# Optimization experiments

Hardware: AMD Instinct MI355X
Metric: run time of the kernel (lower is better)

## Reference

```python
import jax, jax.numpy as jnp
import numpy as np

N_NODES = 50000
N_EDGES = 800000
IN_DIM = 256
OUT_DIM = 256


def setup_inputs() -> dict:
    key = jax.random.key(0)
    k1, k2, k3, k4 = jax.random.split(key, 4)
    feature = jax.random.normal(k1, (N_NODES, IN_DIM), dtype=jnp.float32)
    weight = jax.random.normal(k2, (IN_DIM, OUT_DIM), dtype=jnp.float32)
    src = jax.random.randint(k3, (N_EDGES,), 0, N_NODES, dtype=jnp.int32)
    dst = jax.random.randint(k4, (N_EDGES,), 0, N_NODES, dtype=jnp.int32)
    return {"feature": feature, "weight": weight, "src": src, "dst": dst}


def reference(feature, weight, src, dst):
    # Kernel math: for each edge (s -> d): out[d] += feature[s] @ W.
    # By linearity this equals segment_sum(feature[src] by dst) @ W,
    # which avoids materializing the [E, OUT_DIM] transformed edge features.
    agg = jax.ops.segment_sum(feature[src], dst, num_segments=N_NODES)  # [N, in_dim]
    out = agg @ weight  # [N, out_dim]
    return out
```

## Files before the change

kernel.cpp:

```cpp
#include <hip/hip_runtime.h>
#include <hip/hip_bf16.h>

#define IN_DIM 256
#define OUT_DIM 256
#define CAP 64

typedef __attribute__((ext_vector_type(8))) short bf16x8;
typedef __attribute__((ext_vector_type(4))) float f32x4;


__global__ void feat2bf16(const float* __restrict__ f, unsigned short* __restrict__ o, int n) {
    int i = (blockIdx.x * blockDim.x + threadIdx.x) * 4;
    if (i < n) {
        float4 v = *(const float4*)(f + i);
        __hip_bfloat16 a = __float2bfloat16(v.x), b = __float2bfloat16(v.y);
        __hip_bfloat16 c = __float2bfloat16(v.z), d = __float2bfloat16(v.w);
        ushort4 u;
        u.x = *(unsigned short*)&a; u.y = *(unsigned short*)&b;
        u.z = *(unsigned short*)&c; u.w = *(unsigned short*)&d;
        *(ushort4*)(o + i) = u;
    }
}


__global__ void bucket_kernel(const int* __restrict__ src, const int* __restrict__ dst,
                              int* __restrict__ cursor, int* __restrict__ bucket, int E) {
    int e = blockIdx.x * blockDim.x + threadIdx.x;
    if (e < E) {
        int d = dst[e];
        int pos = atomicAdd(&cursor[d], 1);
        if (pos < CAP) bucket[d * CAP + pos] = src[e];
    }
}


__device__ inline float4 bf4_to_f4(ushort4 u) {
    float4 r;
    r.x = __uint_as_float((unsigned)u.x << 16);
    r.y = __uint_as_float((unsigned)u.y << 16);
    r.z = __uint_as_float((unsigned)u.z << 16);
    r.w = __uint_as_float((unsigned)u.w << 16);
    return r;
}

__global__ void aggregate_bf16(const unsigned short* __restrict__ feat,
                               const int* __restrict__ bucket, const int* __restrict__ cursor,
                               unsigned short* __restrict__ agg, int N) {
    int node = blockIdx.x * 4 + (threadIdx.x >> 6);
    int lane = threadIdx.x & 63;
    if (node >= N) return;
    int cnt = min(cursor[node], CAP);
    const int* bp = bucket + node * CAP;
    float4 a0 = make_float4(0.f,0.f,0.f,0.f), a1 = a0, a2 = a0, a3 = a0;
    int e = 0;
    for (; e + 4 <= cnt; e += 4) {
        int s0 = bp[e], s1 = bp[e+1], s2 = bp[e+2], s3 = bp[e+3];
        ushort4 u0 = ((const ushort4*)(feat + (size_t)s0 * IN_DIM))[lane];
        ushort4 u1 = ((const ushort4*)(feat + (size_t)s1 * IN_DIM))[lane];
        ushort4 u2 = ((const ushort4*)(feat + (size_t)s2 * IN_DIM))[lane];
        ushort4 u3 = ((const ushort4*)(feat + (size_t)s3 * IN_DIM))[lane];
        float4 v0 = bf4_to_f4(u0), v1 = bf4_to_f4(u1), v2 = bf4_to_f4(u2), v3 = bf4_to_f4(u3);
        a0.x += v0.x; a0.y += v0.y; a0.z += v0.z; a0.w += v0.w;
        a1.x += v1.x; a1.y += v1.y; a1.z += v1.z; a1.w += v1.w;
        a2.x += v2.x; a2.y += v2.y; a2.z += v2.z; a2.w += v2.w;
        a3.x += v3.x; a3.y += v3.y; a3.z += v3.z; a3.w += v3.w;
    }
    for (; e < cnt; ++e) {
        int s = bp[e];
        float4 v = bf4_to_f4(((const ushort4*)(feat + (size_t)s * IN_DIM))[lane]);
        a0.x += v.x; a0.y += v.y; a0.z += v.z; a0.w += v.w;
    }
    a0.x += a1.x + a2.x + a3.x;
    a0.y += a1.y + a2.y + a3.y;
    a0.z += a1.z + a2.z + a3.z;
    a0.w += a1.w + a2.w + a3.w;
    __hip_bfloat16 hx = __float2bfloat16(a0.x), hy = __float2bfloat16(a0.y);
    __hip_bfloat16 hz = __float2bfloat16(a0.z), hw = __float2bfloat16(a0.w);
    ushort4 o;
    o.x = *(unsigned short*)&hx; o.y = *(unsigned short*)&hy;
    o.z = *(unsigned short*)&hz; o.w = *(unsigned short*)&hw;
    ((ushort4*)(agg + (size_t)node * IN_DIM))[lane] = o;
}


__global__ void prep_w(const float* __restrict__ W, unsigned short* __restrict__ Wt) {
    int n = blockIdx.x, k = threadIdx.x;
    __hip_bfloat16 h = __float2bfloat16(W[k * OUT_DIM + n]);
    Wt[n * IN_DIM + k] = *(unsigned short*)&h;
}


__global__ __launch_bounds__(256) void gemm_mfma(const unsigned short* __restrict__ A,
                                                 const unsigned short* __restrict__ Bt,
                                                 float* __restrict__ C, int M) {
    __shared__ unsigned short sA[64][40];
    __shared__ unsigned short sB[128][40];
    int tid = threadIdx.x;
    int wave = tid >> 6, lane = tid & 63;
    int m16 = lane & 15, quad = lane >> 4;
    int rb = blockIdx.y * 64, cb = blockIdx.x * 128;
    f32x4 acc[8] = {};

    for (int k0 = 0; k0 < IN_DIM; k0 += 32) {
        {
            int r = tid >> 2, g = tid & 3;
            int gr = rb + r;
            ulonglong2 v; v.x = 0; v.y = 0;
            if (gr < M) v = *(const ulonglong2*)(A + (size_t)gr * IN_DIM + k0 + g * 8);
            *(ulonglong2*)&sA[r][g * 8] = v;
        }
        #pragma unroll
        for (int t = 0; t < 2; ++t) {
            int f = tid + t * 256;
            int nrow = f >> 2, g = f & 3;
            *(ulonglong2*)&sB[nrow][g * 8] =
                *(const ulonglong2*)(Bt + (size_t)(cb + nrow) * IN_DIM + k0 + g * 8);
        }
        __syncthreads();
        bf16x8 afrag = *(const bf16x8*)&sA[wave * 16 + m16][quad * 8];
        #pragma unroll
        for (int nt = 0; nt < 8; ++nt) {
            bf16x8 bfrag = *(const bf16x8*)&sB[nt * 16 + m16][quad * 8];
            acc[nt] = __builtin_amdgcn_mfma_f32_16x16x32_bf16(afrag, bfrag, acc[nt], 0, 0, 0);
        }
        __syncthreads();
    }
    #pragma unroll
    for (int nt = 0; nt < 8; ++nt) {
        #pragma unroll
        for (int r = 0; r < 4; ++r) {
            int gr = rb + wave * 16 + quad * 4 + r;
            if (gr < M) C[(size_t)gr * OUT_DIM + cb + nt * 16 + m16] = acc[nt][r];
        }
    }
}


extern "C" void kernel_launch(void* const* d_in, const int* in_sizes, int n_in,
                              void* d_out, int out_size, void* d_ws, size_t ws_size,
                              hipStream_t stream) {
    const float* feature = (const float*)d_in[0];
    const float* weight  = (const float*)d_in[1];
    const int*   src     = (const int*)d_in[2];
    const int*   dst     = (const int*)d_in[3];
    float*       out     = (float*)d_out;

    int N = in_sizes[0] / IN_DIM;
    int E = in_sizes[2];
    int nfeat = N * IN_DIM;

    char* ws = (char*)d_ws;
    size_t halfTab = (size_t)N * IN_DIM * sizeof(unsigned short);
    unsigned short* agg   = (unsigned short*)ws;
    unsigned short* featb = (unsigned short*)(ws + halfTab);
    unsigned short* Wt    = (unsigned short*)(ws + 2 * halfTab);
    char* p = ws + 2 * halfTab + (size_t)IN_DIM * OUT_DIM * sizeof(unsigned short);
    int* cursor = (int*)p;
    int* bucket = cursor + N;

    hipMemsetAsync(cursor, 0, (size_t)N * sizeof(int), stream);

    feat2bf16<<<(nfeat / 4 + 255) / 256, 256, 0, stream>>>(feature, featb, nfeat);
    prep_w<<<OUT_DIM, IN_DIM, 0, stream>>>(weight, Wt);
    bucket_kernel<<<(E + 255) / 256, 256, 0, stream>>>(src, dst, cursor, bucket, E);
    aggregate_bf16<<<(N + 3) / 4, 256, 0, stream>>>(featb, bucket, cursor, agg, N);

    dim3 ggrid(OUT_DIM / 128, (N + 63) / 64);
    gemm_mfma<<<ggrid, 256, 0, stream>>>(agg, Wt, out, N);
}
```

Before: 224.5 us.

## Fuse prep kernels and column-slice aggregation with 16-bit bucket indices

Merges feature conversion, weight transpose and edge bucketing into one launch, pads per-node cursors to separate cache lines to reduce atomic contention, and stores source indices as 16-bit values. Aggregation now splits the 256 columns into 8 slices of 32, with lane groups striding over edges and a shuffle reduction, so that each slice's gather footprint can stay resident in cache. The 16-bit indices assume fewer than 65536 nodes, and the padded cursor array enlarges the memset.

```diff
diff --git a/kernel.cpp b/kernel.cpp
--- a/kernel.cpp
+++ b/kernel.cpp
@@ -4,89 +4,87 @@
 #define IN_DIM 256
 #define OUT_DIM 256
 #define CAP 64
+#define NS 8
+#define SW 32
 
 typedef __attribute__((ext_vector_type(8))) short bf16x8;
 typedef __attribute__((ext_vector_type(4))) float f32x4;
 
+__device__ inline unsigned short bfbits(float x) {
+    __hip_bfloat16 h = __float2bfloat16(x);
+    return *(unsigned short*)&h;
+}
 
-__global__ void feat2bf16(const float* __restrict__ f, unsigned short* __restrict__ o, int n) {
-    int i = (blockIdx.x * blockDim.x + threadIdx.x) * 4;
-    if (i < n) {
-        float4 v = *(const float4*)(f + i);
-        __hip_bfloat16 a = __float2bfloat16(v.x), b = __float2bfloat16(v.y);
-        __hip_bfloat16 c = __float2bfloat16(v.z), d = __float2bfloat16(v.w);
-        ushort4 u;
-        u.x = *(unsigned short*)&a; u.y = *(unsigned short*)&b;
-        u.z = *(unsigned short*)&c; u.w = *(unsigned short*)&d;
-        *(ushort4*)(o + i) = u;
+
+__global__ void fused_prep(const float* __restrict__ feat, const float* __restrict__ W,
+                           const int* __restrict__ src, const int* __restrict__ dst,
+                           unsigned short* __restrict__ featb, unsigned short* __restrict__ Wt,
+                           int* __restrict__ cursor, unsigned short* __restrict__ bucket,
+                           int E, int nfeat, int EB, int FB) {
+    int b = blockIdx.x, tid = threadIdx.x;
+    if (b < EB) {
+        int e = b * 256 + tid;
+        if (e < E) {
+            int d = dst[e];
+            int pos = atomicAdd(&cursor[d << 4], 1);
+            if (pos < CAP) bucket[d * CAP + pos] = (unsigned short)src[e];
+        }
+    } else if (b < EB + FB) {
+        int i = ((b - EB) * 256 + tid) * 4;
+        if (i < nfeat) {
+            float4 v = *(const float4*)(feat + i);
+            ushort4 u;
+            u.x = bfbits(v.x); u.y = bfbits(v.y); u.z = bfbits(v.z); u.w = bfbits(v.w);
+            *(ushort4*)(featb + i) = u;
+        }
+    } else {
+        int n = b - EB - FB;
+        Wt[n * IN_DIM + tid] = bfbits(W[tid * OUT_DIM + n]);
     }
 }
 
 
-__global__ void bucket_kernel(const int* __restrict__ src, const int* __restrict__ dst,
-                              int* __restrict__ cursor, int* __restrict__ bucket, int E) {
-    int e = blockIdx.x * blockDim.x + threadIdx.x;
-    if (e < E) {
-        int d = dst[e];
-        int pos = atomicAdd(&cursor[d], 1);
-        if (pos < CAP) bucket[d * CAP + pos] = src[e];
+__global__ __launch_bounds__(256) void aggregate_sliced(const unsigned short* __restrict__ featb,
+                                                        const unsigned short* __restrict__ bucket,
+                                                        const int* __restrict__ cursor,
+                                                        unsigned short* __restrict__ agg, int N) {
+    int slice = blockIdx.x & (NS - 1);
+    int nodeblock = blockIdx.x >> 3;
+    int tid = threadIdx.x;
+    int wave = tid >> 6, lane = tid & 63;
+    int grp = lane >> 4, c16 = lane & 15;
+    int colbase = slice * SW + c16 * 2;
+
+    #pragma unroll
+    for (int i = 0; i < 4; ++i) {
+        int node = nodeblock * 16 + wave * 4 + i;
+        if (node >= N) return;
+        int cnt = min(cursor[node << 4], CAP);
+        const unsigned short* bp = bucket + node * CAP;
+        float ax = 0.f, ay = 0.f;
+        int e = grp;
+        for (; e + 4 < cnt; e += 8) {
+            int s0 = bp[e], s1 = bp[e + 4];
+            unsigned u0 = *(const unsigned*)(featb + (size_t)s0 * IN_DIM + colbase);
+            unsigned u1 = *(const unsigned*)(featb + (size_t)s1 * IN_DIM + colbase);
+            ax += __uint_as_float((u0 & 0xFFFFu) << 16);
+            ay += __uint_as_float(u0 & 0xFFFF0000u);
+            ax += __uint_as_float((u1 & 0xFFFFu) << 16);
+            ay += __uint_as_float(u1 & 0xFFFF0000u);
+        }
+        if (e < cnt) {
+            int s = bp[e];
+            unsigned u = *(const unsigned*)(featb + (size_t)s * IN_DIM + colbase);
+            ax += __uint_as_float((u & 0xFFFFu) << 16);
+            ay += __uint_as_float(u & 0xFFFF0000u);
+        }
+        ax += __shfl_xor(ax, 16, 64); ax += __shfl_xor(ax, 32, 64);
+        ay += __shfl_xor(ay, 16, 64); ay += __shfl_xor(ay, 32, 64);
+        if (grp == 0) {
+            ushort2 o; o.x = bfbits(ax); o.y = bfbits(ay);
+            *(ushort2*)(agg + (size_t)node * IN_DIM + colbase) = o;
+        }
     }
-}
-
-
-__device__ inline float4 bf4_to_f4(ushort4 u) {
-    float4 r;
-    r.x = __uint_as_float((unsigned)u.x << 16);
-    r.y = __uint_as_float((unsigned)u.y << 16);
-    r.z = __uint_as_float((unsigned)u.z << 16);
-    r.w = __uint_as_float((unsigned)u.w << 16);
-    return r;
-}
-
-__global__ void aggregate_bf16(const unsigned short* __restrict__ feat,
-                               const int* __restrict__ bucket, const int* __restrict__ cursor,
-                               unsigned short* __restrict__ agg, int N) {
-    int node = blockIdx.x * 4 + (threadIdx.x >> 6);
-    int lane = threadIdx.x & 63;
-    if (node >= N) return;
-    int cnt = min(cursor[node], CAP);
-    const int* bp = bucket + node * CAP;
-    float4 a0 = make_float4(0.f,0.f,0.f,0.f), a1 = a0, a2 = a0, a3 = a0;
-    int e = 0;
-    for (; e + 4 <= cnt; e += 4) {
-        int s0 = bp[e], s1 = bp[e+1], s2 = bp[e+2], s3 = bp[e+3];
-        ushort4 u0 = ((const ushort4*)(feat + (size_t)s0 * IN_DIM))[lane];
-        ushort4 u1 = ((const ushort4*)(feat + (size_t)s1 * IN_DIM))[lane];
-        ushort4 u2 = ((const ushort4*)(feat + (size_t)s2 * IN_DIM))[lane];
-        ushort4 u3 = ((const ushort4*)(feat + (size_t)s3 * IN_DIM))[lane];
-        float4 v0 = bf4_to_f4(u0), v1 = bf4_to_f4(u1), v2 = bf4_to_f4(u2), v3 = bf4_to_f4(u3);
-        a0.x += v0.x; a0.y += v0.y; a0.z += v0.z; a0.w += v0.w;
-        a1.x += v1.x; a1.y += v1.y; a1.z += v1.z; a1.w += v1.w;
-        a2.x += v2.x; a2.y += v2.y; a2.z += v2.z; a2.w += v2.w;
-        a3.x += v3.x; a3.y += v3.y; a3.z += v3.z; a3.w += v3.w;
-    }
-    for (; e < cnt; ++e) {
-        int s = bp[e];
-        float4 v = bf4_to_f4(((const ushort4*)(feat + (size_t)s * IN_DIM))[lane]);
-        a0.x += v.x; a0.y += v.y; a0.z += v.z; a0.w += v.w;
-    }
-    a0.x += a1.x + a2.x + a3.x;
-    a0.y += a1.y + a2.y + a3.y;
-    a0.z += a1.z + a2.z + a3.z;
-    a0.w += a1.w + a2.w + a3.w;
-    __hip_bfloat16 hx = __float2bfloat16(a0.x), hy = __float2bfloat16(a0.y);
-    __hip_bfloat16 hz = __float2bfloat16(a0.z), hw = __float2bfloat16(a0.w);
-    ushort4 o;
-    o.x = *(unsigned short*)&hx; o.y = *(unsigned short*)&hy;
-    o.z = *(unsigned short*)&hz; o.w = *(unsigned short*)&hw;
-    ((ushort4*)(agg + (size_t)node * IN_DIM))[lane] = o;
-}
-
-
-__global__ void prep_w(const float* __restrict__ W, unsigned short* __restrict__ Wt) {
-    int n = blockIdx.x, k = threadIdx.x;
-    __hip_bfloat16 h = __float2bfloat16(W[k * OUT_DIM + n]);
-    Wt[n * IN_DIM + k] = *(unsigned short*)&h;
 }
 
 
@@ -156,14 +154,18 @@
     unsigned short* Wt    = (unsigned short*)(ws + 2 * halfTab);
     char* p = ws + 2 * halfTab + (size_t)IN_DIM * OUT_DIM * sizeof(unsigned short);
     int* cursor = (int*)p;
-    int* bucket = cursor + N;
+    unsigned short* bucket = (unsigned short*)(p + (size_t)N * 16 * sizeof(int));
 
-    hipMemsetAsync(cursor, 0, (size_t)N * sizeof(int), stream);
+    hipMemsetAsync(cursor, 0, (size_t)N * 16 * sizeof(int), stream);
 
-    feat2bf16<<<(nfeat / 4 + 255) / 256, 256, 0, stream>>>(feature, featb, nfeat);
-    prep_w<<<OUT_DIM, IN_DIM, 0, stream>>>(weight, Wt);
-    bucket_kernel<<<(E + 255) / 256, 256, 0, stream>>>(src, dst, cursor, bucket, E);
-    aggregate_bf16<<<(N + 3) / 4, 256, 0, stream>>>(featb, bucket, cursor, agg, N);
+    int EB = (E + 255) / 256;
+    int FB = (nfeat / 4 + 255) / 256;
+    int WB = OUT_DIM;
+    fused_prep<<<EB + FB + WB, 256, 0, stream>>>(feature, weight, src, dst,
+                                                 featb, Wt, cursor, bucket, E, nfeat, EB, FB);
+
+    int nodeblocks = (N + 15) / 16;
+    aggregate_sliced<<<nodeblocks * NS, 256, 0, stream>>>(featb, bucket, cursor, agg, N);
 
     dim3 ggrid(OUT_DIM / 128, (N + 63) / 64);
     gemm_mfma<<<ggrid, 256, 0, stream>>>(agg, Wt, out, N);
```

New measurement: 287.9 us. +28.2%, slower.
